# Kernel optimization log

Measured on AMD Instinct MI355X. Metric: run time of the kernel, lower is better.

The kernel has to match this reference:

```python
import jax, jax.numpy as jnp
import numpy as np

N, E, G = 20000, 320000, 32


def setup_inputs() -> dict:
    key = jax.random.key(0)
    ks = list(jax.random.split(key, 16))
    def nrm(i, shape, s):
        return jax.random.normal(ks[i], shape, jnp.float32) * s
    inp = {}
    inp['x'] = nrm(0, (N, 768), 1.0)
    inp['edge_index'] = jax.random.randint(ks[1], (2, E), 0, N)
    inp['batch'] = jnp.sort(jax.random.randint(ks[2], (N,), 0, G))
    # xavier-ish scales
    inp['proj_w'] = nrm(3, (768, 768), 0.036); inp['proj_b'] = jnp.zeros((768,), jnp.float32)
    inp['gat1_w'] = nrm(4, (768, 1024), 0.033)
    inp['att1_src'] = nrm(5, (4, 256), 0.06); inp['att1_dst'] = nrm(6, (4, 256), 0.06)
    inp['gat1_b'] = jnp.zeros((1024,), jnp.float32)
    inp['ln1_g'] = jnp.ones((1024,), jnp.float32); inp['ln1_b'] = jnp.zeros((1024,), jnp.float32)
    inp['gat2_w'] = nrm(7, (1024, 1024), 0.031)
    inp['att2_src'] = nrm(8, (4, 256), 0.06); inp['att2_dst'] = nrm(9, (4, 256), 0.06)
    inp['gat2_b'] = jnp.zeros((1024,), jnp.float32)
    inp['ln2_g'] = jnp.ones((1024,), jnp.float32); inp['ln2_b'] = jnp.zeros((1024,), jnp.float32)
    inp['gat3_w'] = nrm(10, (1024, 256), 0.04)
    inp['att3_src'] = nrm(11, (1, 256), 0.08); inp['att3_dst'] = nrm(12, (1, 256), 0.08)
    inp['gat3_b'] = jnp.zeros((256,), jnp.float32)
    inp['ln3_g'] = jnp.ones((256,), jnp.float32); inp['ln3_b'] = jnp.zeros((256,), jnp.float32)
    inp['cls1_w'] = nrm(13, (768, 128), 0.047); inp['cls1_b'] = jnp.zeros((128,), jnp.float32)
    inp['cls2_w'] = nrm(14, (128, 1), 0.12); inp['cls2_b'] = jnp.zeros((1,), jnp.float32)
    return inp


def layer_norm(x, g, b, eps=1e-5):
    mu = x.mean(-1, keepdims=True)
    v = ((x - mu) ** 2).mean(-1, keepdims=True)
    return (x - mu) * jax.lax.rsqrt(v + eps) * g + b


def gat_conv(x, src, dst, W, a_src, a_dst, bias, concat):
    # PyG GATConv (eval mode): linear -> per-head additive attention ->
    # segment softmax over incoming edges of each dst node -> scatter-sum.
    n = x.shape[0]
    H, C = a_src.shape
    h = (x @ W).reshape(n, H, C)                      # [N,H,C]
    e_s = (h * a_src[None]).sum(-1)                   # [N,H]
    e_d = (h * a_dst[None]).sum(-1)                   # [N,H]
    logits = jax.nn.leaky_relu(e_s[src] + e_d[dst], 0.2)   # [Etot,H]
    m = jax.ops.segment_max(logits, dst, num_segments=n)   # self-loops -> no empty segments
    ex = jnp.exp(logits - m[dst])
    den = jax.ops.segment_sum(ex, dst, num_segments=n)
    alpha = ex / (den[dst] + 1e-16)                   # [Etot,H]
    out = jax.ops.segment_sum(h[src] * alpha[:, :, None], dst, num_segments=n)  # [N,H,C]
    out = out.reshape(n, H * C) if concat else out.mean(axis=1)
    return out + bias


def reference(x, edge_index, batch, proj_w, proj_b,
              gat1_w, att1_src, att1_dst, gat1_b, ln1_g, ln1_b,
              gat2_w, att2_src, att2_dst, gat2_b, ln2_g, ln2_b,
              gat3_w, att3_src, att3_dst, gat3_b, ln3_g, ln3_b,
              cls1_w, cls1_b, cls2_w, cls2_b):
    n = x.shape[0]
    loop = jnp.arange(n)
    src = jnp.concatenate([edge_index[0], loop])  # GATConv adds self-loops
    dst = jnp.concatenate([edge_index[1], loop])
    h = jax.nn.elu(x @ proj_w + proj_b)
    x1 = jax.nn.elu(layer_norm(gat_conv(h, src, dst, gat1_w, att1_src, att1_dst, gat1_b, True), ln1_g, ln1_b))
    x2 = jax.nn.elu(layer_norm(gat_conv(x1, src, dst, gat2_w, att2_src, att2_dst, gat2_b, True), ln2_g, ln2_b)) + x1
    x3 = jax.nn.elu(layer_norm(gat_conv(x2, src, dst, gat3_w, att3_src, att3_dst, gat3_b, False), ln3_g, ln3_b))
    cnt = jax.ops.segment_sum(jnp.ones((n, 1), x3.dtype), batch, num_segments=G)
    s = jax.ops.segment_sum(x3, batch, num_segments=G)
    mean = s / jnp.maximum(cnt, 1.0)
    mx = jax.ops.segment_max(x3, batch, num_segments=G)
    pooled = jnp.concatenate([mean, mx, s], axis=1)   # [G, 3*256]
    out = jax.nn.relu(pooled @ cls1_w + cls1_b) @ cls2_w + cls2_b
    return out.reshape(-1)
```

## Files before the change

### kernel.cpp

```cpp
#include <hip/hip_runtime.h>
#include <math.h>

typedef float floatx4 __attribute__((ext_vector_type(4)));
typedef _Float16 f16x8 __attribute__((ext_vector_type(8)));
typedef _Float16 f16x4 __attribute__((ext_vector_type(4)));

__device__ __forceinline__ unsigned encf(float f) {
    unsigned u = __float_as_uint(f);
    return (u & 0x80000000u) ? ~u : (u | 0x80000000u);
}
__device__ __forceinline__ float decf(unsigned u) {
    u = (u & 0x80000000u) ? (u & 0x7FFFFFFFu) : ~u;
    return __uint_as_float(u);
}

__global__ __launch_bounds__(256) void cvt_f16_kernel(
    const float* __restrict__ in, _Float16* __restrict__ out, size_t n4)
{
    size_t i = (size_t)blockIdx.x * 256 + threadIdx.x;
    if (i >= n4) return;
    float4 v = ((const float4*)in)[i];
    f16x4 o;
    o[0] = (_Float16)v.x; o[1] = (_Float16)v.y; o[2] = (_Float16)v.z; o[3] = (_Float16)v.w;
    ((f16x4*)out)[i] = o;
}

__global__ __launch_bounds__(256) void wt_kernel(
    const float* __restrict__ w, _Float16* __restrict__ wt, int K, int N)
{
    __shared__ float t[32][33];
    int bx = blockIdx.x * 32, by = blockIdx.y * 32;
    int tx = threadIdx.x & 31, ty = threadIdx.x >> 5;
    for (int r = ty; r < 32; r += 8)
        t[r][tx] = w[(size_t)(by + r) * N + bx + tx];
    __syncthreads();
    for (int r = ty; r < 32; r += 8)
        wt[(size_t)(bx + r) * K + by + tx] = (_Float16)t[tx][r];
}

__global__ __launch_bounds__(256) void gemm_f16(
    const _Float16* __restrict__ A, const _Float16* __restrict__ BT,
    const float* __restrict__ bias, _Float16* __restrict__ C,
    int M, int K, int N, int act)
{
    __shared__ _Float16 Al[128 * 32];
    __shared__ _Float16 Bl[128 * 32];
    int tid = threadIdx.x;
    int lane = tid & 63, wave = tid >> 6;
    int row0 = blockIdx.y * 128, col0 = blockIdx.x * 128;
    int wm = (wave >> 1) * 64, wn = (wave & 1) * 64;
    int l15 = lane & 15, quad = lane >> 4;

    int sr0 = tid >> 2, sc = (tid & 3) * 8;
    int sr1 = sr0 + 64;
    int ar0 = row0 + sr0; if (ar0 > M - 1) ar0 = M - 1;
    int ar1 = row0 + sr1; if (ar1 > M - 1) ar1 = M - 1;
    const _Float16* Ap0 = A + (size_t)ar0 * K + sc;
    const _Float16* Ap1 = A + (size_t)ar1 * K + sc;
    const _Float16* Bp0 = BT + (size_t)(col0 + sr0) * K + sc;
    const _Float16* Bp1 = BT + (size_t)(col0 + sr1) * K + sc;

    floatx4 acc[4][4] = {};

    for (int k0 = 0; k0 < K; k0 += 32) {
        f16x8 a0 = *(const f16x8*)(Ap0 + k0);
        f16x8 a1 = *(const f16x8*)(Ap1 + k0);
        f16x8 b0 = *(const f16x8*)(Bp0 + k0);
        f16x8 b1 = *(const f16x8*)(Bp1 + k0);
        __syncthreads();
        *(f16x8*)&Al[sr0 * 32 + sc] = a0;
        *(f16x8*)&Al[sr1 * 32 + sc] = a1;
        *(f16x8*)&Bl[sr0 * 32 + sc] = b0;
        *(f16x8*)&Bl[sr1 * 32 + sc] = b1;
        __syncthreads();
        f16x8 af[4], bfr[4];
        #pragma unroll
        for (int i = 0; i < 4; i++) {
            af[i]  = *(const f16x8*)&Al[(wm + i * 16 + l15) * 32 + quad * 8];
            bfr[i] = *(const f16x8*)&Bl[(wn + i * 16 + l15) * 32 + quad * 8];
        }
        #pragma unroll
        for (int i = 0; i < 4; i++)
            #pragma unroll
            for (int j = 0; j < 4; j++)
                acc[i][j] = __builtin_amdgcn_mfma_f32_16x16x32_f16(af[i], bfr[j], acc[i][j], 0, 0, 0);
    }

    #pragma unroll
    for (int i = 0; i < 4; i++) {
        #pragma unroll
        for (int v = 0; v < 4; v++) {
            int gr = row0 + wm + i * 16 + quad * 4 + v;
            if (gr >= M) continue;
            #pragma unroll
            for (int j = 0; j < 4; j++) {
                int gc = col0 + wn + j * 16 + l15;
                float val = acc[i][j][v];
                if (bias) val += bias[gc];
                if (act) val = val > 0.f ? val : (expf(val) - 1.f);
                C[(size_t)gr * N + gc] = (_Float16)val;
            }
        }
    }
}

__global__ __launch_bounds__(256) void attn_scores_kernel(
    const _Float16* __restrict__ h, const float* __restrict__ asrc, const float* __restrict__ adst,
    float* __restrict__ es, float* __restrict__ ed, int Nn, int H)
{
    int wid = (blockIdx.x * 256 + threadIdx.x) >> 6;
    int lane = threadIdx.x & 63;
    if (wid >= Nn * H) return;
    int node = wid / H, hh = wid % H;
    const _Float16* hp = h + (size_t)node * H * 256 + hh * 256 + lane * 4;
    f16x4 v = *(const f16x4*)hp;
    float ss = 0.f, sd = 0.f;
    #pragma unroll
    for (int j = 0; j < 4; j++) {
        float f = (float)v[j];
        ss = fmaf(f, asrc[hh * 256 + lane * 4 + j], ss);
        sd = fmaf(f, adst[hh * 256 + lane * 4 + j], sd);
    }
    #pragma unroll
    for (int o = 32; o; o >>= 1) { ss += __shfl_down(ss, o); sd += __shfl_down(sd, o); }
    if (lane == 0) { es[wid] = ss; ed[wid] = sd; }
}

__global__ __launch_bounds__(256) void csr_init(int* __restrict__ deg, int Nn) {
    int i = blockIdx.x * 256 + threadIdx.x;
    if (i < Nn) deg[i] = 1;
}
__global__ __launch_bounds__(256) void csr_count(const int* __restrict__ ei, int* __restrict__ deg, int E) {
    int i = blockIdx.x * 256 + threadIdx.x;
    if (i < E) atomicAdd(&deg[ei[E + i]], 1);
}
__global__ __launch_bounds__(256) void scan1(const int* __restrict__ deg, int* __restrict__ incl,
                                             int* __restrict__ bsums, int Nn) {
    __shared__ int sd[256];
    int idx = blockIdx.x * 256 + threadIdx.x;
    sd[threadIdx.x] = (idx < Nn) ? deg[idx] : 0;
    __syncthreads();
    for (int o = 1; o < 256; o <<= 1) {
        int x = (threadIdx.x >= (unsigned)o) ? sd[threadIdx.x - o] : 0;
        __syncthreads();
        sd[threadIdx.x] += x;
        __syncthreads();
    }
    if (idx < Nn) incl[idx] = sd[threadIdx.x];
    if (threadIdx.x == 255) bsums[blockIdx.x] = sd[255];
}
__global__ void scan2(int* __restrict__ bsums, int nb) {
    if (blockIdx.x == 0 && threadIdx.x == 0) {
        int run = 0;
        for (int i = 0; i < nb; i++) { int v = bsums[i]; bsums[i] = run; run += v; }
    }
}
__global__ __launch_bounds__(256) void scan3(const int* __restrict__ incl, const int* __restrict__ deg,
                                             const int* __restrict__ bsums, int* __restrict__ rowstart,
                                             int* __restrict__ cursor, int Nn) {
    int idx = blockIdx.x * 256 + threadIdx.x;
    if (idx >= Nn) return;
    int rs = incl[idx] - deg[idx] + bsums[blockIdx.x];
    rowstart[idx] = rs;
    cursor[idx] = rs;
}
__global__ __launch_bounds__(256) void csr_fill(const int* __restrict__ ei, int* __restrict__ cursor,
                                                int* __restrict__ csrc, int E, int Nn) {
    int i = blockIdx.x * 256 + threadIdx.x;
    if (i >= E + Nn) return;
    int s, d;
    if (i < E) { s = ei[i]; d = ei[E + i]; } else { s = d = i - E; }
    int pos = atomicAdd(&cursor[d], 1);
    csrc[pos] = s;
}

template<int H>
__global__ __launch_bounds__(64 * H) void gat_aggregate(
    const int* __restrict__ rowstart, const int* __restrict__ deg,
    const int* __restrict__ csrc,
    const float* __restrict__ es, const float* __restrict__ ed,
    const _Float16* __restrict__ h, _Float16* __restrict__ out)
{
    constexpr int T = 64 * H;
    constexpr int NW = T / 64;
    int d = blockIdx.x;
    int t = threadIdx.x;
    int lane = t & 63, wave = t >> 6;
    int head = t & (H - 1);
    int slot = t / H;
    int st = rowstart[d], dg = deg[d];

    __shared__ float red[NW][H];
    __shared__ float mh[H], zh[H];

    float edv = ed[d * H + head];
    float m = -1e30f;
    for (int j = slot; j < dg; j += 64) {
        int s = csrc[st + j];
        float l = es[s * H + head] + edv;
        l = l > 0.f ? l : 0.2f * l;
        m = fmaxf(m, l);
    }
    #pragma unroll
    for (int o = H; o < 64; o <<= 1) m = fmaxf(m, __shfl_xor(m, o));
    if (NW > 1) {
        if (lane < H) red[wave][head] = m;
        __syncthreads();
        m = red[0][head];
        #pragma unroll
        for (int w2 = 1; w2 < NW; w2++) m = fmaxf(m, red[w2][head]);
        __syncthreads();
    }
    float z = 0.f;
    for (int j = slot; j < dg; j += 64) {
        int s = csrc[st + j];
        float l = es[s * H + head] + edv;
        l = l > 0.f ? l : 0.2f * l;
        z += expf(l - m);
    }
    #pragma unroll
    for (int o = H; o < 64; o <<= 1) z += __shfl_xor(z, o);
    if (NW > 1) {
        if (lane < H) red[wave][head] = z;
        __syncthreads();
        z = 0.f;
        #pragma unroll
        for (int w2 = 0; w2 < NW; w2++) z += red[w2][head];
    }
    if (t < H) { mh[t] = m; zh[t] = z; }
    __syncthreads();

    int head2 = t >> 6;
    float m2 = mh[head2];
    float rden = 1.f / (zh[head2] + 1e-16f);
    float ed2 = ed[d * H + head2];
    float acc0 = 0.f, acc1 = 0.f, acc2 = 0.f, acc3 = 0.f;
    const _Float16* hb = h + (size_t)t * 4;
    int HC = T * 4;
    for (int j = 0; j < dg; j++) {
        int s = csrc[st + j];
        float l = es[s * H + head2] + ed2;
        l = l > 0.f ? l : 0.2f * l;
        float a = expf(l - m2) * rden;
        f16x4 v = *(const f16x4*)(hb + (size_t)s * HC);
        acc0 = fmaf(a, (float)v[0], acc0);
        acc1 = fmaf(a, (float)v[1], acc1);
        acc2 = fmaf(a, (float)v[2], acc2);
        acc3 = fmaf(a, (float)v[3], acc3);
    }
    f16x4 o;
    o[0] = (_Float16)acc0; o[1] = (_Float16)acc1; o[2] = (_Float16)acc2; o[3] = (_Float16)acc3;
    *(f16x4*)(out + (size_t)d * HC + t * 4) = o;
}

__global__ __launch_bounds__(256) void ln_elu_kernel(
    const _Float16* __restrict__ agg, const float* __restrict__ bias,
    const float* __restrict__ gam, const float* __restrict__ bet,
    const float* resid, float* out, _Float16* out16, int HC)
{
    int row = blockIdx.x;
    int tid = threadIdx.x;
    int per = HC >> 8;
    float vr[4];
    const _Float16* ap = agg + (size_t)row * HC;
    float sum = 0.f;
    for (int i = 0; i < per; i++) {
        int c = i * 256 + tid;
        float x = (float)ap[c] + bias[c];
        vr[i] = x; sum += x;
    }
    __shared__ float sm[4];
    #pragma unroll
    for (int o = 32; o; o >>= 1) sum += __shfl_down(sum, o);
    if ((tid & 63) == 0) sm[tid >> 6] = sum;
    __syncthreads();
    float mean = (sm[0] + sm[1] + sm[2] + sm[3]) / (float)HC;
    float sq = 0.f;
    for (int i = 0; i < per; i++) { float dd = vr[i] - mean; sq = fmaf(dd, dd, sq); }
    __syncthreads();
    #pragma unroll
    for (int o = 32; o; o >>= 1) sq += __shfl_down(sq, o);
    if ((tid & 63) == 0) sm[tid >> 6] = sq;
    __syncthreads();
    float var = (sm[0] + sm[1] + sm[2] + sm[3]) / (float)HC;
    float rstd = rsqrtf(var + 1e-5f);
    for (int i = 0; i < per; i++) {
        int c = i * 256 + tid;
        float y = (vr[i] - mean) * rstd * gam[c] + bet[c];
        y = y > 0.f ? y : (expf(y) - 1.f);
        if (resid) y += resid[(size_t)row * HC + c];
        out[(size_t)row * HC + c] = y;
        if (out16) out16[(size_t)row * HC + c] = (_Float16)y;
    }
}

__global__ __launch_bounds__(256) void pool_kernel(
    const float* __restrict__ x3, const int* __restrict__ batch,
    float* __restrict__ ps, unsigned* __restrict__ pm, int* __restrict__ cnt, int Nn)
{
    int c = threadIdx.x;
    int n0 = blockIdx.x * 16;
    int end = n0 + 16; if (end > Nn) end = Nn;
    if (n0 >= Nn) return;
    int curg = batch[n0];
    float s = 0.f, m = -1e30f; int k = 0;
    for (int n = n0; n < end; n++) {
        int g = batch[n];
        if (g != curg) {
            atomicAdd(&ps[curg * 256 + c], s);
            atomicMax(&pm[curg * 256 + c], encf(m));
            if (c == 0) atomicAdd(&cnt[curg], k);
            s = 0.f; m = -1e30f; k = 0; curg = g;
        }
        float v = x3[(size_t)n * 256 + c];
        s += v; m = fmaxf(m, v); k++;
    }
    atomicAdd(&ps[curg * 256 + c], s);
    atomicMax(&pm[curg * 256 + c], encf(m));
    if (c == 0) atomicAdd(&cnt[curg], k);
}

__global__ __launch_bounds__(128) void classifier_kernel(
    const float* __restrict__ ps, const unsigned* __restrict__ pm, const int* __restrict__ cnt,
    const float* __restrict__ w1, const float* __restrict__ b1,
    const float* __restrict__ w2, const float* __restrict__ b2, float* __restrict__ out)
{
    int g = blockIdx.x;
    int tid = threadIdx.x;
    __shared__ float pooled[768];
    __shared__ float red[2];
    float c = (float)cnt[g];
    if (c < 1.f) c = 1.f;
    for (int i = tid; i < 256; i += 128) {
        float s = ps[g * 256 + i];
        pooled[i] = s / c;
        pooled[256 + i] = decf(pm[g * 256 + i]);
        pooled[512 + i] = s;
    }
    __syncthreads();
    float acc = b1[tid];
    for (int k = 0; k < 768; k++) acc = fmaf(pooled[k], w1[k * 128 + tid], acc);
    acc = fmaxf(acc, 0.f);
    float v = acc * w2[tid];
    #pragma unroll
    for (int o = 32; o; o >>= 1) v += __shfl_down(v, o);
    if ((tid & 63) == 0) red[tid >> 6] = v;
    __syncthreads();
    if (tid == 0) out[g] = red[0] + red[1] + b2[0];
}

extern "C" void kernel_launch(void* const* d_in, const int* in_sizes, int n_in,
                              void* d_out, int out_size, void* d_ws, size_t ws_size,
                              hipStream_t stream)
{
    const float* x      = (const float*)d_in[0];
    const int*   ei     = (const int*)d_in[1];
    const int*   batch  = (const int*)d_in[2];
    const float* proj_w = (const float*)d_in[3];
    const float* proj_b = (const float*)d_in[4];
    const float* gat1_w = (const float*)d_in[5];
    const float* att1_s = (const float*)d_in[6];
    const float* att1_d = (const float*)d_in[7];
    const float* gat1_b = (const float*)d_in[8];
    const float* ln1_g  = (const float*)d_in[9];
    const float* ln1_b  = (const float*)d_in[10];
    const float* gat2_w = (const float*)d_in[11];
    const float* att2_s = (const float*)d_in[12];
    const float* att2_d = (const float*)d_in[13];
    const float* gat2_b = (const float*)d_in[14];
    const float* ln2_g  = (const float*)d_in[15];
    const float* ln2_b  = (const float*)d_in[16];
    const float* gat3_w = (const float*)d_in[17];
    const float* att3_s = (const float*)d_in[18];
    const float* att3_d = (const float*)d_in[19];
    const float* gat3_b = (const float*)d_in[20];
    const float* ln3_g  = (const float*)d_in[21];
    const float* ln3_b  = (const float*)d_in[22];
    const float* cls1_w = (const float*)d_in[23];
    const float* cls1_b = (const float*)d_in[24];
    const float* cls2_w = (const float*)d_in[25];
    const float* cls2_b = (const float*)d_in[26];

    int Nn = in_sizes[0] / 768;
    int E  = in_sizes[1] / 2;
    int Gg = out_size;
    int Etot = E + Nn;
    int nb  = (Nn + 255) / 256;

    char* w = (char*)d_ws;
    size_t NB16 = (size_t)Nn * 1024 * sizeof(_Float16);
    size_t NB32 = (size_t)Nn * 1024 * sizeof(float);
    _Float16* P = (_Float16*)(w);
    _Float16* Q = (_Float16*)(w + NB16);
    _Float16* R = (_Float16*)(w + 2 * NB16);
    float*  X = (float*)(w + 3 * NB16);
    char* p = w + 3 * NB16 + NB32;
    _Float16* projT = (_Float16*)p; p += (size_t)768 * 768 * 2;
    _Float16* g1T   = (_Float16*)p; p += (size_t)1024 * 768 * 2;
    _Float16* g2T   = (_Float16*)p; p += (size_t)1024 * 1024 * 2;
    _Float16* g3T   = (_Float16*)p; p += (size_t)256 * 1024 * 2;
    float*    es    = (float*)p;  p += (size_t)Nn * 4 * 4;
    float*    ed_   = (float*)p;  p += (size_t)Nn * 4 * 4;
    int*      deg   = (int*)p;    p += (size_t)Nn * 4;
    int*      incl  = (int*)p;    p += (size_t)Nn * 4;
    int*      rowst = (int*)p;    p += (size_t)Nn * 4;
    int*      curs  = (int*)p;    p += (size_t)Nn * 4;
    int*      bsums = (int*)p;    p += (size_t)nb * 4 + 64;
    int*      csrc  = (int*)p;    p += (size_t)Etot * 4;
    float*    ps    = (float*)p;  p += (size_t)Gg * 256 * 4;
    unsigned* pm    = (unsigned*)p; p += (size_t)Gg * 256 * 4;
    int*      cnt   = (int*)p;    p += 256;

    dim3 blk(256);

    wt_kernel<<<dim3(768 / 32, 768 / 32), blk, 0, stream>>>(proj_w, projT, 768, 768);
    wt_kernel<<<dim3(1024 / 32, 768 / 32), blk, 0, stream>>>(gat1_w, g1T, 768, 1024);
    wt_kernel<<<dim3(1024 / 32, 1024 / 32), blk, 0, stream>>>(gat2_w, g2T, 1024, 1024);
    wt_kernel<<<dim3(256 / 32, 1024 / 32), blk, 0, stream>>>(gat3_w, g3T, 1024, 256);

    {
        size_t n4 = (size_t)Nn * 768 / 4;
        cvt_f16_kernel<<<dim3((unsigned)((n4 + 255) / 256)), blk, 0, stream>>>(x, P, n4);
    }

    csr_init<<<dim3(nb), blk, 0, stream>>>(deg, Nn);
    csr_count<<<dim3((E + 255) / 256), blk, 0, stream>>>(ei, deg, E);
    scan1<<<dim3(nb), blk, 0, stream>>>(deg, incl, bsums, Nn);
    scan2<<<dim3(1), dim3(64), 0, stream>>>(bsums, nb);
    scan3<<<dim3(nb), blk, 0, stream>>>(incl, deg, bsums, rowst, curs, Nn);
    csr_fill<<<dim3((Etot + 255) / 256), blk, 0, stream>>>(ei, curs, csrc, E, Nn);

    int mg = (Nn + 127) / 128;

    gemm_f16<<<dim3(768 / 128, mg), blk, 0, stream>>>(P, projT, proj_b, Q, Nn, 768, 768, 1);

    auto run_gat = [&](const _Float16* xin16, const _Float16* WT, const float* as_, const float* ad_,
                       const float* gb, const float* lg, const float* lb, const float* resid,
                       _Float16* hbuf, _Float16* aggbuf, float* xout, _Float16* xout16,
                       int K, int H, int C) {
        int HC = H * C;
        gemm_f16<<<dim3(HC / 128, mg), blk, 0, stream>>>(xin16, WT, nullptr, hbuf, Nn, K, HC, 0);
        int nw = Nn * H;
        attn_scores_kernel<<<dim3((nw + 3) / 4), blk, 0, stream>>>(hbuf, as_, ad_, es, ed_, Nn, H);
        if (H == 4)
            gat_aggregate<4><<<dim3(Nn), dim3(256), 0, stream>>>(rowst, deg, csrc, es, ed_, hbuf, aggbuf);
        else
            gat_aggregate<1><<<dim3(Nn), dim3(64), 0, stream>>>(rowst, deg, csrc, es, ed_, hbuf, aggbuf);
        ln_elu_kernel<<<dim3(Nn), blk, 0, stream>>>(aggbuf, gb, lg, lb, resid, xout, xout16, HC);
    };

    run_gat(Q, g1T, att1_s, att1_d, gat1_b, ln1_g, ln1_b, nullptr, P, R, X, Q, 768, 4, 256);
    run_gat(Q, g2T, att2_s, att2_d, gat2_b, ln2_g, ln2_b, X, P, R, X, Q, 1024, 4, 256);
    run_gat(Q, g3T, att3_s, att3_d, gat3_b, ln3_g, ln3_b, nullptr, P, R, X, nullptr, 1024, 1, 256);

    hipMemsetAsync(ps, 0, (size_t)Gg * 256 * 4, stream);
    hipMemsetAsync(pm, 0, (size_t)Gg * 256 * 4, stream);
    hipMemsetAsync(cnt, 0, (size_t)Gg * 4, stream);
    pool_kernel<<<dim3((Nn + 15) / 16), blk, 0, stream>>>(X, batch, ps, pm, cnt, Nn);
    classifier_kernel<<<dim3(Gg), dim3(128), 0, stream>>>(ps, pm, cnt, cls1_w, cls1_b, cls2_w, cls2_b, (float*)d_out);
}
```

Baseline: 942.7 us.

## Use direct global-to-LDS loads in GEMM and split GAT aggregation into stages

The GEMM tile loads now go straight from global memory into LDS through global_load_lds, so the A and B data no longer pass through registers. A barrier moves to the end of each k step so the next loads cannot overwrite tiles still being read. The GAT aggregation is split into three kernels: a wave-per-node segment max and sum, a per-edge kernel that writes normalized attention weights (this needs a new cdst array), and a gather kernel that prefetches the source index and weight of the next edge. This removes the per-block barriers and the repeated exp work from the gather, at the cost of extra launches and an Etot×H weight buffer written and read back through global memory.

```diff
diff --git a/kernel.cpp b/kernel.cpp
--- a/kernel.cpp
+++ b/kernel.cpp
@@ -12,6 +12,11 @@
 __device__ __forceinline__ float decf(unsigned u) {
     u = (u & 0x80000000u) ? (u & 0x7FFFFFFFu) : ~u;
     return __uint_as_float(u);
+}
+__device__ __forceinline__ void glds16(const void* g, void* l) {
+    __builtin_amdgcn_global_load_lds(
+        (const __attribute__((address_space(1))) unsigned int*)g,
+        (__attribute__((address_space(3))) unsigned int*)l, 16, 0, 0);
 }
 
 __global__ __launch_bounds__(256) void cvt_f16_kernel(
@@ -51,27 +56,28 @@
     int wm = (wave >> 1) * 64, wn = (wave & 1) * 64;
     int l15 = lane & 15, quad = lane >> 4;
 
-    int sr0 = tid >> 2, sc = (tid & 3) * 8;
-    int sr1 = sr0 + 64;
-    int ar0 = row0 + sr0; if (ar0 > M - 1) ar0 = M - 1;
-    int ar1 = row0 + sr1; if (ar1 > M - 1) ar1 = M - 1;
-    const _Float16* Ap0 = A + (size_t)ar0 * K + sc;
-    const _Float16* Ap1 = A + (size_t)ar1 * K + sc;
-    const _Float16* Bp0 = BT + (size_t)(col0 + sr0) * K + sc;
-    const _Float16* Bp1 = BT + (size_t)(col0 + sr1) * K + sc;
+    int rg0 = wave * 2, rg1 = rg0 + 1;
+    int srow0 = rg0 * 16 + (lane >> 2);
+    int srow1 = rg1 * 16 + (lane >> 2);
+    int scol = (lane & 3) * 8;
+    int arow0 = row0 + srow0; if (arow0 > M - 1) arow0 = M - 1;
+    int arow1 = row0 + srow1; if (arow1 > M - 1) arow1 = M - 1;
+    const _Float16* gA0 = A + (size_t)arow0 * K + scol;
+    const _Float16* gA1 = A + (size_t)arow1 * K + scol;
+    const _Float16* gB0 = BT + (size_t)(col0 + srow0) * K + scol;
+    const _Float16* gB1 = BT + (size_t)(col0 + srow1) * K + scol;
+    _Float16* lA0 = &Al[rg0 * 512];
+    _Float16* lA1 = &Al[rg1 * 512];
+    _Float16* lB0 = &Bl[rg0 * 512];
+    _Float16* lB1 = &Bl[rg1 * 512];
 
     floatx4 acc[4][4] = {};
 
     for (int k0 = 0; k0 < K; k0 += 32) {
-        f16x8 a0 = *(const f16x8*)(Ap0 + k0);
-        f16x8 a1 = *(const f16x8*)(Ap1 + k0);
-        f16x8 b0 = *(const f16x8*)(Bp0 + k0);
-        f16x8 b1 = *(const f16x8*)(Bp1 + k0);
-        __syncthreads();
-        *(f16x8*)&Al[sr0 * 32 + sc] = a0;
-        *(f16x8*)&Al[sr1 * 32 + sc] = a1;
-        *(f16x8*)&Bl[sr0 * 32 + sc] = b0;
-        *(f16x8*)&Bl[sr1 * 32 + sc] = b1;
+        glds16(gA0 + k0, lA0);
+        glds16(gA1 + k0, lA1);
+        glds16(gB0 + k0, lB0);
+        glds16(gB1 + k0, lB1);
         __syncthreads();
         f16x8 af[4], bfr[4];
         #pragma unroll
@@ -84,6 +90,7 @@
             #pragma unroll
             for (int j = 0; j < 4; j++)
                 acc[i][j] = __builtin_amdgcn_mfma_f32_16x16x32_f16(af[i], bfr[j], acc[i][j], 0, 0, 0);
+        __syncthreads();
     }
 
     #pragma unroll
@@ -165,89 +172,102 @@
     cursor[idx] = rs;
 }
 __global__ __launch_bounds__(256) void csr_fill(const int* __restrict__ ei, int* __restrict__ cursor,
-                                                int* __restrict__ csrc, int E, int Nn) {
+                                                int* __restrict__ csrc, int* __restrict__ cdst,
+                                                int E, int Nn) {
     int i = blockIdx.x * 256 + threadIdx.x;
     if (i >= E + Nn) return;
     int s, d;
     if (i < E) { s = ei[i]; d = ei[E + i]; } else { s = d = i - E; }
     int pos = atomicAdd(&cursor[d], 1);
     csrc[pos] = s;
+    cdst[pos] = d;
 }
 
 template<int H>
-__global__ __launch_bounds__(64 * H) void gat_aggregate(
+__global__ __launch_bounds__(256) void seg_mz(
     const int* __restrict__ rowstart, const int* __restrict__ deg,
-    const int* __restrict__ csrc,
+    const int* __restrict__ csrc, const float* __restrict__ es,
+    const float* __restrict__ ed, float2* __restrict__ mz, int Nn)
+{
+    int d = (blockIdx.x * 256 + threadIdx.x) >> 6;
+    int lane = threadIdx.x & 63;
+    if (d >= Nn) return;
+    constexpr int S = 64 / H;
+    int head = lane & (H - 1);
+    int slot = lane / H;
+    int st = rowstart[d], dg = deg[d];
+    float edv = ed[d * H + head];
+    float m = -1e30f;
+    for (int j = slot; j < dg; j += S) {
+        float l = es[csrc[st + j] * H + head] + edv;
+        l = l > 0.f ? l : 0.2f * l;
+        m = fmaxf(m, l);
+    }
+    #pragma unroll
+    for (int o = H; o < 64; o <<= 1) m = fmaxf(m, __shfl_xor(m, o));
+    float z = 0.f;
+    for (int j = slot; j < dg; j += S) {
+        float l = es[csrc[st + j] * H + head] + edv;
+        l = l > 0.f ? l : 0.2f * l;
+        z += expf(l - m);
+    }
+    #pragma unroll
+    for (int o = H; o < 64; o <<= 1) z += __shfl_xor(z, o);
+    if (lane < H) mz[d * H + lane] = make_float2(m, 1.f / (z + 1e-16f));
+}
+
+template<int H>
+__global__ __launch_bounds__(256) void edge_alpha(
+    const int* __restrict__ csrc, const int* __restrict__ cdst,
     const float* __restrict__ es, const float* __restrict__ ed,
+    const float2* __restrict__ mz, float* __restrict__ wse, int Etot)
+{
+    int i = blockIdx.x * 256 + threadIdx.x;
+    if (i >= Etot) return;
+    int s = csrc[i], d = cdst[i];
+    float a[H];
+    #pragma unroll
+    for (int hh = 0; hh < H; hh++) {
+        float l = es[s * H + hh] + ed[d * H + hh];
+        l = l > 0.f ? l : 0.2f * l;
+        float2 mzv = mz[d * H + hh];
+        a[hh] = expf(l - mzv.x) * mzv.y;
+    }
+    #pragma unroll
+    for (int hh = 0; hh < H; hh++) wse[(size_t)i * H + hh] = a[hh];
+}
+
+template<int H>
+__global__ __launch_bounds__(64 * H) void gat_gather(
+    const int* __restrict__ rowstart, const int* __restrict__ deg,
+    const int* __restrict__ csrc, const float* __restrict__ wse,
     const _Float16* __restrict__ h, _Float16* __restrict__ out)
 {
     constexpr int T = 64 * H;
-    constexpr int NW = T / 64;
+    const int HC = T * 4;
     int d = blockIdx.x;
     int t = threadIdx.x;
-    int lane = t & 63, wave = t >> 6;
-    int head = t & (H - 1);
-    int slot = t / H;
+    int head2 = t >> 6;
     int st = rowstart[d], dg = deg[d];
-
-    __shared__ float red[NW][H];
-    __shared__ float mh[H], zh[H];
-
-    float edv = ed[d * H + head];
-    float m = -1e30f;
-    for (int j = slot; j < dg; j += 64) {
-        int s = csrc[st + j];
-        float l = es[s * H + head] + edv;
-        l = l > 0.f ? l : 0.2f * l;
-        m = fmaxf(m, l);
-    }
-    #pragma unroll
-    for (int o = H; o < 64; o <<= 1) m = fmaxf(m, __shfl_xor(m, o));
-    if (NW > 1) {
-        if (lane < H) red[wave][head] = m;
-        __syncthreads();
-        m = red[0][head];
-        #pragma unroll
-        for (int w2 = 1; w2 < NW; w2++) m = fmaxf(m, red[w2][head]);
-        __syncthreads();
-    }
-    float z = 0.f;
-    for (int j = slot; j < dg; j += 64) {
-        int s = csrc[st + j];
-        float l = es[s * H + head] + edv;
-        l = l > 0.f ? l : 0.2f * l;
-        z += expf(l - m);
-    }
-    #pragma unroll
-    for (int o = H; o < 64; o <<= 1) z += __shfl_xor(z, o);
-    if (NW > 1) {
-        if (lane < H) red[wave][head] = z;
-        __syncthreads();
-        z = 0.f;
-        #pragma unroll
-        for (int w2 = 0; w2 < NW; w2++) z += red[w2][head];
-    }
-    if (t < H) { mh[t] = m; zh[t] = z; }
-    __syncthreads();
-
-    int head2 = t >> 6;
-    float m2 = mh[head2];
-    float rden = 1.f / (zh[head2] + 1e-16f);
-    float ed2 = ed[d * H + head2];
+    const _Float16* hb = h + (size_t)t * 4;
     float acc0 = 0.f, acc1 = 0.f, acc2 = 0.f, acc3 = 0.f;
-    const _Float16* hb = h + (size_t)t * 4;
-    int HC = T * 4;
-    for (int j = 0; j < dg; j++) {
-        int s = csrc[st + j];
-        float l = es[s * H + head2] + ed2;
-        l = l > 0.f ? l : 0.2f * l;
-        float a = expf(l - m2) * rden;
+    int s = csrc[st];
+    float a = wse[(size_t)st * H + head2];
+    for (int j = 1; j < dg; j++) {
+        int s_n = csrc[st + j];
+        float a_n = wse[(size_t)(st + j) * H + head2];
         f16x4 v = *(const f16x4*)(hb + (size_t)s * HC);
         acc0 = fmaf(a, (float)v[0], acc0);
         acc1 = fmaf(a, (float)v[1], acc1);
         acc2 = fmaf(a, (float)v[2], acc2);
         acc3 = fmaf(a, (float)v[3], acc3);
-    }
+        s = s_n; a = a_n;
+    }
+    f16x4 v = *(const f16x4*)(hb + (size_t)s * HC);
+    acc0 = fmaf(a, (float)v[0], acc0);
+    acc1 = fmaf(a, (float)v[1], acc1);
+    acc2 = fmaf(a, (float)v[2], acc2);
+    acc3 = fmaf(a, (float)v[3], acc3);
     f16x4 o;
     o[0] = (_Float16)acc0; o[1] = (_Float16)acc1; o[2] = (_Float16)acc2; o[3] = (_Float16)acc3;
     *(f16x4*)(out + (size_t)d * HC + t * 4) = o;
@@ -388,28 +408,36 @@
     int nb  = (Nn + 255) / 256;
 
     char* w = (char*)d_ws;
+    size_t off = 0;
+    auto alloc = [&](size_t bytes) -> char* {
+        char* r = w + off;
+        off += (bytes + 255) & ~(size_t)255;
+        return r;
+    };
     size_t NB16 = (size_t)Nn * 1024 * sizeof(_Float16);
     size_t NB32 = (size_t)Nn * 1024 * sizeof(float);
-    _Float16* P = (_Float16*)(w);
-    _Float16* Q = (_Float16*)(w + NB16);
-    _Float16* R = (_Float16*)(w + 2 * NB16);
-    float*  X = (float*)(w + 3 * NB16);
-    char* p = w + 3 * NB16 + NB32;
-    _Float16* projT = (_Float16*)p; p += (size_t)768 * 768 * 2;
-    _Float16* g1T   = (_Float16*)p; p += (size_t)1024 * 768 * 2;
-    _Float16* g2T   = (_Float16*)p; p += (size_t)1024 * 1024 * 2;
-    _Float16* g3T   = (_Float16*)p; p += (size_t)256 * 1024 * 2;
-    float*    es    = (float*)p;  p += (size_t)Nn * 4 * 4;
-    float*    ed_   = (float*)p;  p += (size_t)Nn * 4 * 4;
-    int*      deg   = (int*)p;    p += (size_t)Nn * 4;
-    int*      incl  = (int*)p;    p += (size_t)Nn * 4;
-    int*      rowst = (int*)p;    p += (size_t)Nn * 4;
-    int*      curs  = (int*)p;    p += (size_t)Nn * 4;
-    int*      bsums = (int*)p;    p += (size_t)nb * 4 + 64;
-    int*      csrc  = (int*)p;    p += (size_t)Etot * 4;
-    float*    ps    = (float*)p;  p += (size_t)Gg * 256 * 4;
-    unsigned* pm    = (unsigned*)p; p += (size_t)Gg * 256 * 4;
-    int*      cnt   = (int*)p;    p += 256;
+    _Float16* P = (_Float16*)alloc(NB16);
+    _Float16* Q = (_Float16*)alloc(NB16);
+    _Float16* R = (_Float16*)alloc(NB16);
+    float*  X = (float*)alloc(NB32);
+    _Float16* projT = (_Float16*)alloc((size_t)768 * 768 * 2);
+    _Float16* g1T   = (_Float16*)alloc((size_t)1024 * 768 * 2);
+    _Float16* g2T   = (_Float16*)alloc((size_t)1024 * 1024 * 2);
+    _Float16* g3T   = (_Float16*)alloc((size_t)256 * 1024 * 2);
+    float*    es    = (float*)alloc((size_t)Nn * 4 * 4);
+    float*    ed_   = (float*)alloc((size_t)Nn * 4 * 4);
+    float2*   mz    = (float2*)alloc((size_t)Nn * 4 * 8);
+    int*      deg   = (int*)alloc((size_t)Nn * 4);
+    int*      incl  = (int*)alloc((size_t)Nn * 4);
+    int*      rowst = (int*)alloc((size_t)Nn * 4);
+    int*      curs  = (int*)alloc((size_t)Nn * 4);
+    int*      bsums = (int*)alloc((size_t)nb * 4);
+    int*      csrc  = (int*)alloc((size_t)Etot * 4);
+    int*      cdst  = (int*)alloc((size_t)Etot * 4);
+    float*    wse   = (float*)alloc((size_t)Etot * 4 * 4);
+    float*    ps    = (float*)alloc((size_t)Gg * 256 * 4);
+    unsigned* pm    = (unsigned*)alloc((size_t)Gg * 256 * 4);
+    int*      cnt   = (int*)alloc(256);
 
     dim3 blk(256);
 
@@ -428,7 +456,7 @@
     scan1<<<dim3(nb), blk, 0, stream>>>(deg, incl, bsums, Nn);
     scan2<<<dim3(1), dim3(64), 0, stream>>>(bsums, nb);
     scan3<<<dim3(nb), blk, 0, stream>>>(incl, deg, bsums, rowst, curs, Nn);
-    csr_fill<<<dim3((Etot + 255) / 256), blk, 0, stream>>>(ei, curs, csrc, E, Nn);
+    csr_fill<<<dim3((Etot + 255) / 256), blk, 0, stream>>>(ei, curs, csrc, cdst, E, Nn);
 
     int mg = (Nn + 127) / 128;
 
@@ -442,10 +470,15 @@
         gemm_f16<<<dim3(HC / 128, mg), blk, 0, stream>>>(xin16, WT, nullptr, hbuf, Nn, K, HC, 0);
         int nw = Nn * H;
         attn_scores_kernel<<<dim3((nw + 3) / 4), blk, 0, stream>>>(hbuf, as_, ad_, es, ed_, Nn, H);
-        if (H == 4)
-            gat_aggregate<4><<<dim3(Nn), dim3(256), 0, stream>>>(rowst, deg, csrc, es, ed_, hbuf, aggbuf);
-        else
-            gat_aggregate<1><<<dim3(Nn), dim3(64), 0, stream>>>(rowst, deg, csrc, es, ed_, hbuf, aggbuf);
+        if (H == 4) {
+            seg_mz<4><<<dim3((Nn + 3) / 4), blk, 0, stream>>>(rowst, deg, csrc, es, ed_, mz, Nn);
+            edge_alpha<4><<<dim3((Etot + 255) / 256), blk, 0, stream>>>(csrc, cdst, es, ed_, mz, wse, Etot);
+            gat_gather<4><<<dim3(Nn), dim3(256), 0, stream>>>(rowst, deg, csrc, wse, hbuf, aggbuf);
+        } else {
+            seg_mz<1><<<dim3((Nn + 3) / 4), blk, 0, stream>>>(rowst, deg, csrc, es, ed_, mz, Nn);
+            edge_alpha<1><<<dim3((Etot + 255) / 256), blk, 0, stream>>>(csrc, cdst, es, ed_, mz, wse, Etot);
+            gat_gather<1><<<dim3(Nn), dim3(64), 0, stream>>>(rowst, deg, csrc, wse, hbuf, aggbuf);
+        }
         ln_elu_kernel<<<dim3(Nn), blk, 0, stream>>>(aggbuf, gb, lg, lb, resid, xout, xout16, HC);
     };
 
```

New measurement: 926.8 us. Within noise of the previous version (-1.7%).
